# Kernel optimization log

Hardware: AMD Instinct MI355X
Metric: run time of the kernel (lower is better)

Reference implementation:

```python
import jax, jax.numpy as jnp
import numpy as np

IN_DIM = 128
LAYER_DIMS = [128, 128]
NUM_SAMPLES = [25, 10]
L0 = 3072
NEG_WEIGHT = 1.0


def setup_inputs() -> dict:
    key = jax.random.key(0)
    ks = jax.random.split(key, 12)
    feat = jax.random.normal(ks[0], (L0, IN_DIM), dtype=jnp.float32)
    nodes = jax.random.randint(ks[1], (L0,), 0, L0)
    nb0 = jnp.arange(L0)
    nb1 = jax.random.randint(ks[2], (L0 * 10,), 0, L0)
    nb2 = jax.random.randint(ks[3], (L0 * 10 * 25,), 0, L0)
    src_idx = jax.random.randint(ks[4], (1024,), 0, L0)
    pos_idx = jax.random.randint(ks[5], (1024,), 0, L0)
    neg_idx = jax.random.randint(ks[6], (512,), 0, L0)
    g = 0.05
    # mean aggregator weights: layer0 in=IN_DIM, layer1 in=2*128 (concat)
    w_self_0 = jax.random.normal(ks[7], (IN_DIM, 128), jnp.float32) * g
    w_neigh_0 = jax.random.normal(ks[8], (IN_DIM, 128), jnp.float32) * g
    w_self_1 = jax.random.normal(ks[9], (256, 128), jnp.float32) * g
    w_neigh_1 = jax.random.normal(ks[10], (256, 128), jnp.float32) * g
    return dict(nodes=nodes, feat=feat, src_idx=src_idx, pos_idx=pos_idx,
                neg_idx=neg_idx, nb0=nb0, nb1=nb1, nb2=nb2,
                w_self_0=w_self_0, w_neigh_0=w_neigh_0,
                w_self_1=w_self_1, w_neigh_1=w_neigh_1)


def _aggregate(hidden, params):
    # GraphSAGE layer stack: at layer l, combine each hop with the mean of its
    # sampled neighbors, concat self/neigh transforms, relu except last layer.
    num_layers = len(NUM_SAMPLES)
    for layer in range(num_layers):
        w_self, w_neigh = params[layer]
        is_last = layer == num_layers - 1
        next_hidden = []
        for hop in range(num_layers - layer):
            s = NUM_SAMPLES[num_layers - hop - 1]
            self_v = hidden[hop]  # [n, d]
            neigh = hidden[hop + 1].reshape(self_v.shape[0], s, self_v.shape[1])
            neigh_mean = jnp.mean(neigh, axis=1)
            h = jnp.concatenate([self_v @ w_self, neigh_mean @ w_neigh], axis=1)
            if not is_last:
                h = jax.nn.relu(h)
            next_hidden.append(h)
        hidden = next_hidden
    return hidden[0]


def _l2_normalize(x, eps=1e-12):
    return x * jax.lax.rsqrt(jnp.maximum(jnp.sum(x * x, axis=1, keepdims=True), eps))


def reference(nodes, feat, src_idx, pos_idx, neg_idx, nb0, nb1, nb2,
              w_self_0, w_neigh_0, w_self_1, w_neigh_1):
    hidden = [feat[nb0], feat[nb1], feat[nb2]]
    params = [(w_self_0, w_neigh_0), (w_self_1, w_neigh_1)]
    output = _aggregate(hidden, params)          # [L0, 256]
    output = _l2_normalize(output)
    src_emb = output[src_idx]                    # [B, 256]
    pos_emb = output[pos_idx]
    neg_emb = output[neg_idx]                    # [Nneg, 256]

    aff = jnp.sum(src_emb * pos_emb, axis=1)     # [B]
    neg_aff = src_emb @ neg_emb.T                # [B, Nneg]

    # MRR via double argsort (tf double top_k equivalent; ties -> positive last)
    aff_all = jnp.concatenate([neg_aff, aff[:, None]], axis=1)
    order = jnp.argsort(-aff_all, axis=1, stable=True)
    ranks = jnp.argsort(order, axis=1, stable=True)
    mrr = jnp.mean(1.0 / (ranks[:, -1].astype(jnp.float32) + 1.0))

    # sigmoid cross-entropy: labels 1 -> softplus(-x); labels 0 -> softplus(x)
    true_xent = jax.nn.softplus(-aff)
    neg_xent = jax.nn.softplus(neg_aff)
    loss = jnp.sum(true_xent) + NEG_WEIGHT * jnp.sum(neg_xent)
    loss = loss / jnp.asarray(src_emb.shape[0], jnp.float32)
    return src_emb, loss, mrr
```

## Files before the change

### kernel.cpp

```cpp
#include <hip/hip_runtime.h>
#include <math.h>

#define L0      3072
#define BATCH   1024
#define NNEG    512


__device__ __forceinline__ float bf2f(unsigned short u) {
  return __uint_as_float(((unsigned)u) << 16);
}
__device__ __forceinline__ void store_out(float v, float* p) { *p = v; }
__device__ __forceinline__ void store_out(float v, unsigned short* p) {
  unsigned x = __float_as_uint(v);
  *p = (unsigned short)((x + 0x7fff + ((x >> 16) & 1)) >> 16);
}

template<int K, int AW, int HOFF, bool NORM, typename OutT>
__global__ __launch_bounds__(512) void k_mm(
    const float* __restrict__ Ain,
    const float* __restrict__ W0, const float* __restrict__ W1,
    OutT* __restrict__ Out, const int ldo, const int outHalfOff) {
  __shared__ float AT[6 * AW];
  __shared__ float rs[8][3];
  const int t = threadIdx.x;
  const int base = blockIdx.x * 6;
  {
    const float4* __restrict__ src = (const float4*)(Ain + base * AW);
    float4* __restrict__ dst = (float4*)AT;
    for (int idx = t; idx < 6 * AW / 4; idx += 512) dst[idx] = src[idx];
  }
  __syncthreads();

  const int wave = t >> 6;
  const int half = wave >> 2;
  const int colg = (wave >> 1) & 1;
  const int rowg = wave & 1;
  const int rg = rowg * 3;
  const int col = colg * 64 + (t & 63);
  const float* __restrict__ W = (half ? W1 : W0) + col;
  const float* __restrict__ A0 = AT + rg * AW + half * HOFF;

  float acc[3] = {0.f, 0.f, 0.f};
#pragma unroll 4
  for (int d = 0; d < K; d += 4) {
    float4 a[3];
#pragma unroll
    for (int r = 0; r < 3; ++r) a[r] = *(const float4*)&A0[r * AW + d];
    float w[4];
#pragma unroll
    for (int i2 = 0; i2 < 4; ++i2) w[i2] = W[(d + i2) * 128];
#pragma unroll
    for (int i2 = 0; i2 < 4; ++i2)
#pragma unroll
      for (int r = 0; r < 3; ++r)
        acc[r] = fmaf(((const float*)&a[r])[i2], w[i2], acc[r]);
  }

  float scale[3] = {1.f, 1.f, 1.f};
  if (NORM) {
    float p[3];
#pragma unroll
    for (int r = 0; r < 3; ++r) p[r] = acc[r] * acc[r];
#pragma unroll
    for (int off = 32; off > 0; off >>= 1)
#pragma unroll
      for (int r = 0; r < 3; ++r) p[r] += __shfl_xor(p[r], off, 64);
    if ((t & 63) == 0) { rs[wave][0] = p[0]; rs[wave][1] = p[1]; rs[wave][2] = p[2]; }
    __syncthreads();
#pragma unroll
    for (int r = 0; r < 3; ++r) {
      const float s = rs[rowg][r] + rs[rowg + 2][r] + rs[rowg + 4][r] + rs[rowg + 6][r];
      scale[r] = rsqrtf(fmaxf(s, 1e-12f));
    }
  }
  OutT* __restrict__ O = Out + half * outHalfOff;
#pragma unroll
  for (int r = 0; r < 3; ++r)
    store_out(acc[r] * scale[r], &O[(base + rg + r) * ldo + col]);
}

__global__ __launch_bounds__(512) void k_aggmm(
    const unsigned short* __restrict__ X0, const unsigned short* __restrict__ Y0,
    const int* __restrict__ nb0, const int* __restrict__ nb1,
    const int* __restrict__ nb2,
    const float* __restrict__ ws1, const float* __restrict__ wn1,
    float* __restrict__ R) {
  __shared__ float gB[40][128], gC[40][128], gD[40][128];
  __shared__ float HT[4 * 512];
  __shared__ float rs[8][2];
  const int t = threadIdx.x;
  const int wave = t >> 6, lam = t & 63;
  const int base = blockIdx.x * 4;
  const int c8 = lam & 15, sub = lam >> 4;

#pragma unroll
  for (int k = 0; k < 5; ++k) {
    const int tau = wave + k * 8;
    const int li = tau / 10, j = tau - li * 10;
    const int r = (base + li) * 10 + j;
    int myidx = 0;
    if (lam < 25) myidx = nb2[r * 25 + lam];
    else if (lam == 25) myidx = nb1[r];

    float d8[8];
#pragma unroll
    for (int e = 0; e < 8; ++e) d8[e] = 0.f;
#pragma unroll
    for (int m = 0; m < 7; ++m) {
      const int kk = sub + 4 * m;
      const int ridx = __shfl(myidx, kk, 64);
      if (kk < 25) {
        const float4 raw = *(const float4*)(Y0 + ridx * 128 + c8 * 8);
        const unsigned short* u = (const unsigned short*)&raw;
#pragma unroll
        for (int e = 0; e < 8; ++e) d8[e] += bf2f(u[e]);
      }
    }
#pragma unroll
    for (int e = 0; e < 8; ++e) d8[e] += __shfl_xor(d8[e], 16, 64);
#pragma unroll
    for (int e = 0; e < 8; ++e) d8[e] += __shfl_xor(d8[e], 32, 64);

    const int r1 = __shfl(myidx, 25, 64);
    if (sub == 0) {
#pragma unroll
      for (int e = 0; e < 8; ++e) gD[tau][c8 * 8 + e] = fmaxf(d8[e] * 0.04f, 0.f);
      const float4 raw = *(const float4*)(Y0 + r1 * 128 + c8 * 8);
      const unsigned short* u = (const unsigned short*)&raw;
#pragma unroll
      for (int e = 0; e < 8; ++e) gB[tau][c8 * 8 + e] = bf2f(u[e]);
    } else if (sub == 1) {
      const float4 raw = *(const float4*)(X0 + r1 * 128 + c8 * 8);
      const unsigned short* u = (const unsigned short*)&raw;
#pragma unroll
      for (int e = 0; e < 8; ++e) gC[tau][c8 * 8 + e] = fmaxf(bf2f(u[e]), 0.f);
    }
  }
  __syncthreads();

  {
    const int li = t >> 7, c = t & 127;
    const int n0 = nb0[base + li];
    float sB = 0.f, sC = 0.f, sD = 0.f;
#pragma unroll
    for (int jj = 0; jj < 10; ++jj) {
      sB += gB[li * 10 + jj][c];
      sC += gC[li * 10 + jj][c];
      sD += gD[li * 10 + jj][c];
    }
    HT[li * 512 + c]       = fmaxf(bf2f(X0[n0 * 128 + c]), 0.f);
    HT[li * 512 + 128 + c] = fmaxf(sB * 0.1f, 0.f);
    HT[li * 512 + 256 + c] = sC * 0.1f;
    HT[li * 512 + 384 + c] = sD * 0.1f;
  }
  __syncthreads();

  const int half = wave >> 2;
  const int colg = (wave >> 1) & 1;
  const int rowg = wave & 1;
  const int rg = rowg * 2;
  const int col = colg * 64 + lam;
  const float* __restrict__ W = (half ? wn1 : ws1) + col;
  const float* __restrict__ A0 = HT + rg * 512 + half * 256;

  float acc[2] = {0.f, 0.f};
#pragma unroll 4
  for (int d = 0; d < 256; d += 4) {
    float4 a[2];
#pragma unroll
    for (int r = 0; r < 2; ++r) a[r] = *(const float4*)&A0[r * 512 + d];
    float w[4];
#pragma unroll
    for (int i2 = 0; i2 < 4; ++i2) w[i2] = W[(d + i2) * 128];
#pragma unroll
    for (int i2 = 0; i2 < 4; ++i2)
#pragma unroll
      for (int r = 0; r < 2; ++r)
        acc[r] = fmaf(((const float*)&a[r])[i2], w[i2], acc[r]);
  }

  float p[2];
#pragma unroll
  for (int r = 0; r < 2; ++r) p[r] = acc[r] * acc[r];
#pragma unroll
  for (int off = 32; off > 0; off >>= 1)
#pragma unroll
    for (int r = 0; r < 2; ++r) p[r] += __shfl_xor(p[r], off, 64);
  if (lam == 0) { rs[wave][0] = p[0]; rs[wave][1] = p[1]; }
  __syncthreads();
#pragma unroll
  for (int r = 0; r < 2; ++r) {
    const float s = rs[rowg][r] + rs[rowg + 2][r] + rs[rowg + 4][r] + rs[rowg + 6][r];
    const float scale = rsqrtf(fmaxf(s, 1e-12f));
    R[(base + rg + r) * 256 + half * 128 + col] = acc[r] * scale;
  }
}

__device__ __forceinline__ float softplusf(float x) {
  return fmaxf(x, 0.f) + log1pf(expf(-fabsf(x)));
}

__global__ __launch_bounds__(512) void k_neg(
    const float* __restrict__ O,
    const int* __restrict__ src_idx, const int* __restrict__ pos_idx,
    const int* __restrict__ neg_idx,
    float* __restrict__ out_src, int* __restrict__ rankPart,
    float* __restrict__ spPosPart, float* __restrict__ spNegPart) {
  __shared__ float SP[64 * 260];
  __shared__ float BT[256 * 64];
  __shared__ float affL[32];
  __shared__ int cntL[32];
  __shared__ float wsum[16];
  const int t = threadIdx.x;
  const int bid = blockIdx.x;
  const int rowBase = (bid >> 3) * 32;
  const int colBase = (bid & 7) * 64;
  const bool first = ((bid & 7) == 0);

  {
    const float4* __restrict__ s4 = (const float4*)O;
#pragma unroll
    for (int idx = t; idx < 64 * 64; idx += 512) {
      const int row = idx >> 6, c4 = idx & 63;
      const int rid = (row < 32) ? src_idx[rowBase + row]
                                 : pos_idx[rowBase + row - 32];
      *(float4*)&SP[row * 260 + c4 * 4] = s4[rid * 64 + c4];
    }
  }
  {
    const float4* __restrict__ s4 = (const float4*)O;
#pragma unroll
    for (int idx = t; idx < 64 * 64; idx += 512) {
      const int j = idx & 63, c4 = idx >> 6;
      const float4 v = s4[neg_idx[colBase + j] * 64 + c4];
      BT[(4 * c4 + 0) * 64 + j] = v.x;
      BT[(4 * c4 + 1) * 64 + j] = v.y;
      BT[(4 * c4 + 2) * 64 + j] = v.z;
      BT[(4 * c4 + 3) * 64 + j] = v.w;
    }
  }
  if (first) {
    const float4* __restrict__ s4 = (const float4*)O;
    float4* __restrict__ d4o = (float4*)out_src;
#pragma unroll
    for (int idx = t; idx < 32 * 64; idx += 512) {
      const int rr = idx >> 6, c4 = idx & 63;
      d4o[(rowBase + rr) * 64 + c4] = s4[src_idx[rowBase + rr] * 64 + c4];
    }
  }
  __syncthreads();

  const int tc = t & 31;
  const int rowg = t >> 5;
  const float* __restrict__ A0 = SP + rowg * 260;
  const float* __restrict__ A1 = SP + (rowg + 16) * 260;
  const float* __restrict__ SV = SP + t * 260;
  const float* __restrict__ PV = SP + (32 + t) * 260;

  float acc00 = 0.f, acc01 = 0.f, acc10 = 0.f, acc11 = 0.f, aff = 0.f;
#pragma unroll 4
  for (int d4 = 0; d4 < 64; ++d4) {
    const int dd = d4 * 4;
    const float4 a0 = *(const float4*)&A0[dd];
    const float4 a1 = *(const float4*)&A1[dd];
    float2 b[4];
#pragma unroll
    for (int i2 = 0; i2 < 4; ++i2)
      b[i2] = *(const float2*)&BT[(dd + i2) * 64 + 2 * tc];
    float4 sv, pv;
    if (t < 32) {
      sv = *(const float4*)&SV[dd];
      pv = *(const float4*)&PV[dd];
    }
#pragma unroll
    for (int i2 = 0; i2 < 4; ++i2) {
      const float va0 = ((const float*)&a0)[i2];
      const float va1 = ((const float*)&a1)[i2];
      acc00 = fmaf(va0, b[i2].x, acc00);
      acc01 = fmaf(va0, b[i2].y, acc01);
      acc10 = fmaf(va1, b[i2].x, acc10);
      acc11 = fmaf(va1, b[i2].y, acc11);
      if (t < 32)
        aff = fmaf(((const float*)&sv)[i2], ((const float*)&pv)[i2], aff);
    }
  }
  if (t < 32) affL[t] = aff;
  __syncthreads();

  float sp = softplusf(acc00) + softplusf(acc01) +
             softplusf(acc10) + softplusf(acc11);
  const float av0 = affL[rowg], av1 = affL[rowg + 16];
  int c0 = ((acc00 >= av0) ? 1 : 0) + ((acc01 >= av0) ? 1 : 0);
  int c1 = ((acc10 >= av1) ? 1 : 0) + ((acc11 >= av1) ? 1 : 0);
#pragma unroll
  for (int off = 16; off > 0; off >>= 1) {
    sp += __shfl_down(sp, off, 32);
    c0 += __shfl_down(c0, off, 32);
    c1 += __shfl_down(c1, off, 32);
  }
  if ((t & 31) == 0) {
    cntL[rowg] = c0;
    cntL[rowg + 16] = c1;
    wsum[rowg] = sp;
  }
  __syncthreads();

  if (t < 32) rankPart[(bid & 7) * 1024 + rowBase + t] = cntL[t];
  if (t == 0) {
    float sn = 0.f;
#pragma unroll
    for (int w = 0; w < 16; ++w) sn += wsum[w];
    spNegPart[bid] = sn;
  }
  if (first && t == 0) {
    float ps = 0.f;
#pragma unroll
    for (int r = 0; r < 32; ++r) ps += softplusf(-affL[r]);
    spPosPart[bid >> 3] = ps;
  }
}

__global__ __launch_bounds__(256) void k_finalize(
    const int* __restrict__ rankPart, const float* __restrict__ spPosPart,
    const float* __restrict__ spNegPart, float* __restrict__ out) {
  __shared__ float wa[4], wb[4];
  const int t = threadIdx.x;
  float s = 0.f;
  for (int i = t; i < BATCH; i += 256) {
    int rv = 0;
#pragma unroll
    for (int p = 0; p < 8; ++p) rv += rankPart[p * 1024 + i];
    s += 1.f / (float)(rv + 1);
  }
  float l = 0.f;
  if (t < 256) l += spNegPart[t];
  if (t < 32) l += spPosPart[t];
#pragma unroll
  for (int off = 32; off > 0; off >>= 1) {
    s += __shfl_down(s, off, 64);
    l += __shfl_down(l, off, 64);
  }
  if ((t & 63) == 0) { wa[t >> 6] = s; wb[t >> 6] = l; }
  __syncthreads();
  if (t == 0) {
    out[BATCH * 256]     = (wb[0] + wb[1] + wb[2] + wb[3]) * (1.f / 1024.f);
    out[BATCH * 256 + 1] = (wa[0] + wa[1] + wa[2] + wa[3]) * (1.f / 1024.f);
  }
}

extern "C" void kernel_launch(void* const* d_in, const int* in_sizes, int n_in,
                              void* d_out, int out_size, void* d_ws, size_t ws_size,
                              hipStream_t stream) {
  const float* feat   = (const float*)d_in[1];
  const int* src_idx  = (const int*)d_in[2];
  const int* pos_idx  = (const int*)d_in[3];
  const int* neg_idx  = (const int*)d_in[4];
  const int* nb0      = (const int*)d_in[5];
  const int* nb1      = (const int*)d_in[6];
  const int* nb2      = (const int*)d_in[7];
  const float* ws0    = (const float*)d_in[8];
  const float* wn0    = (const float*)d_in[9];
  const float* ws1    = (const float*)d_in[10];
  const float* wn1    = (const float*)d_in[11];

  float* wsf = (float*)d_ws;
  unsigned short* X0 = (unsigned short*)d_ws;
  unsigned short* Y0 = X0 + 393216;
  float* R       = wsf + 1966080;
  float* spPosP  = wsf + 2752512;
  float* spNegP  = wsf + 2752640;
  int*   rankP   = (int*)(wsf + 2753664);
  float* out     = (float*)d_out;

  k_mm<128, 128, 0, false, unsigned short><<<L0 / 6, 512, 0, stream>>>(
      feat, ws0, wn0, X0, 128, 393216);
  k_aggmm<<<L0 / 4, 512, 0, stream>>>(
      X0, Y0, nb0, nb1, nb2, ws1, wn1, R);
  k_neg<<<256, 512, 0, stream>>>(
      R, src_idx, pos_idx, neg_idx, out, rankP, spPosP, spNegP);
  k_finalize<<<1, 256, 0, stream>>>(rankP, spPosP, spNegP, out);
}
```

Before: 155.9 us.

## Accumulate neighbor sums in registers and swizzle negative-embedding transpose tile

The aggregation kernel now has each wave accumulate five hop-1 neighbor rows in registers and write only per-wave partial sums to shared memory. This replaces the 40-row staging arrays and the 10-way shared-memory reduction, cutting shared memory use and LDS traffic. Separately, the negative-embedding load in the scoring kernel is changed to coalesced row-major global reads. The transposed tile is stored with an XOR swizzle, and the matmul loop reads with the matching swizzled column to avoid bank conflicts.

```diff
diff --git a/kernel.cpp b/kernel.cpp
--- a/kernel.cpp
+++ b/kernel.cpp
@@ -85,7 +85,7 @@
     const int* __restrict__ nb2,
     const float* __restrict__ ws1, const float* __restrict__ wn1,
     float* __restrict__ R) {
-  __shared__ float gB[40][128], gC[40][128], gD[40][128];
+  __shared__ float pB[8][128], pC[8][128], pD[8][128];
   __shared__ float HT[4 * 512];
   __shared__ float rs[8][2];
   const int t = threadIdx.x;
@@ -93,47 +93,62 @@
   const int base = blockIdx.x * 4;
   const int c8 = lam & 15, sub = lam >> 4;
 
-#pragma unroll
-  for (int k = 0; k < 5; ++k) {
-    const int tau = wave + k * 8;
-    const int li = tau / 10, j = tau - li * 10;
-    const int r = (base + li) * 10 + j;
-    int myidx = 0;
-    if (lam < 25) myidx = nb2[r * 25 + lam];
-    else if (lam == 25) myidx = nb1[r];
-
-    float d8[8];
-#pragma unroll
-    for (int e = 0; e < 8; ++e) d8[e] = 0.f;
-#pragma unroll
-    for (int m = 0; m < 7; ++m) {
-      const int kk = sub + 4 * m;
-      const int ridx = __shfl(myidx, kk, 64);
-      if (kk < 25) {
-        const float4 raw = *(const float4*)(Y0 + ridx * 128 + c8 * 8);
+  {
+    const int li = wave >> 1;
+    const int j0 = (wave & 1) * 5;
+    float Ba[8], Ca[8], Da[8];
+#pragma unroll
+    for (int e = 0; e < 8; ++e) { Ba[e] = 0.f; Ca[e] = 0.f; Da[e] = 0.f; }
+#pragma unroll
+    for (int jj = 0; jj < 5; ++jj) {
+      const int r = (base + li) * 10 + j0 + jj;
+      int myidx = 0;
+      if (lam < 25) myidx = nb2[r * 25 + lam];
+      else if (lam == 25) myidx = nb1[r];
+
+      float d8[8];
+#pragma unroll
+      for (int e = 0; e < 8; ++e) d8[e] = 0.f;
+#pragma unroll
+      for (int m = 0; m < 7; ++m) {
+        const int kk = sub + 4 * m;
+        const int ridx = __shfl(myidx, kk, 64);
+        if (kk < 25) {
+          const float4 raw = *(const float4*)(Y0 + ridx * 128 + c8 * 8);
+          const unsigned short* u = (const unsigned short*)&raw;
+#pragma unroll
+          for (int e = 0; e < 8; ++e) d8[e] += bf2f(u[e]);
+        }
+      }
+#pragma unroll
+      for (int e = 0; e < 8; ++e) d8[e] += __shfl_xor(d8[e], 16, 64);
+#pragma unroll
+      for (int e = 0; e < 8; ++e) d8[e] += __shfl_xor(d8[e], 32, 64);
+#pragma unroll
+      for (int e = 0; e < 8; ++e) Da[e] += fmaxf(d8[e] * 0.04f, 0.f);
+
+      const int r1 = __shfl(myidx, 25, 64);
+      if (sub == 0) {
+        const float4 raw = *(const float4*)(Y0 + r1 * 128 + c8 * 8);
         const unsigned short* u = (const unsigned short*)&raw;
 #pragma unroll
-        for (int e = 0; e < 8; ++e) d8[e] += bf2f(u[e]);
+        for (int e = 0; e < 8; ++e) Ba[e] += bf2f(u[e]);
+      } else if (sub == 1) {
+        const float4 raw = *(const float4*)(X0 + r1 * 128 + c8 * 8);
+        const unsigned short* u = (const unsigned short*)&raw;
+#pragma unroll
+        for (int e = 0; e < 8; ++e) Ca[e] += fmaxf(bf2f(u[e]), 0.f);
       }
     }
-#pragma unroll
-    for (int e = 0; e < 8; ++e) d8[e] += __shfl_xor(d8[e], 16, 64);
-#pragma unroll
-    for (int e = 0; e < 8; ++e) d8[e] += __shfl_xor(d8[e], 32, 64);
-
-    const int r1 = __shfl(myidx, 25, 64);
     if (sub == 0) {
 #pragma unroll
-      for (int e = 0; e < 8; ++e) gD[tau][c8 * 8 + e] = fmaxf(d8[e] * 0.04f, 0.f);
-      const float4 raw = *(const float4*)(Y0 + r1 * 128 + c8 * 8);
-      const unsigned short* u = (const unsigned short*)&raw;
-#pragma unroll
-      for (int e = 0; e < 8; ++e) gB[tau][c8 * 8 + e] = bf2f(u[e]);
+      for (int e = 0; e < 8; ++e) {
+        pD[wave][c8 * 8 + e] = Da[e];
+        pB[wave][c8 * 8 + e] = Ba[e];
+      }
     } else if (sub == 1) {
-      const float4 raw = *(const float4*)(X0 + r1 * 128 + c8 * 8);
-      const unsigned short* u = (const unsigned short*)&raw;
-#pragma unroll
-      for (int e = 0; e < 8; ++e) gC[tau][c8 * 8 + e] = fmaxf(bf2f(u[e]), 0.f);
+#pragma unroll
+      for (int e = 0; e < 8; ++e) pC[wave][c8 * 8 + e] = Ca[e];
     }
   }
   __syncthreads();
@@ -141,13 +156,9 @@
   {
     const int li = t >> 7, c = t & 127;
     const int n0 = nb0[base + li];
-    float sB = 0.f, sC = 0.f, sD = 0.f;
-#pragma unroll
-    for (int jj = 0; jj < 10; ++jj) {
-      sB += gB[li * 10 + jj][c];
-      sC += gC[li * 10 + jj][c];
-      sD += gD[li * 10 + jj][c];
-    }
+    const float sB = pB[li * 2][c] + pB[li * 2 + 1][c];
+    const float sC = pC[li * 2][c] + pC[li * 2 + 1][c];
+    const float sD = pD[li * 2][c] + pD[li * 2 + 1][c];
     HT[li * 512 + c]       = fmaxf(bf2f(X0[n0 * 128 + c]), 0.f);
     HT[li * 512 + 128 + c] = fmaxf(sB * 0.1f, 0.f);
     HT[li * 512 + 256 + c] = sC * 0.1f;
@@ -231,12 +242,13 @@
     const float4* __restrict__ s4 = (const float4*)O;
 #pragma unroll
     for (int idx = t; idx < 64 * 64; idx += 512) {
-      const int j = idx & 63, c4 = idx >> 6;
+      const int j = idx >> 6, c4 = idx & 63;
       const float4 v = s4[neg_idx[colBase + j] * 64 + c4];
-      BT[(4 * c4 + 0) * 64 + j] = v.x;
-      BT[(4 * c4 + 1) * 64 + j] = v.y;
-      BT[(4 * c4 + 2) * 64 + j] = v.z;
-      BT[(4 * c4 + 3) * 64 + j] = v.w;
+      const int js = j ^ ((c4 & 31) << 1);
+      BT[(4 * c4 + 0) * 64 + js] = v.x;
+      BT[(4 * c4 + 1) * 64 + js] = v.y;
+      BT[(4 * c4 + 2) * 64 + js] = v.z;
+      BT[(4 * c4 + 3) * 64 + js] = v.w;
     }
   }
   if (first) {
@@ -261,12 +273,14 @@
 #pragma unroll 4
   for (int d4 = 0; d4 < 64; ++d4) {
     const int dd = d4 * 4;
+    const int g = (d4 & 31) << 1;
+    const int bcol = (2 * tc) ^ g;
     const float4 a0 = *(const float4*)&A0[dd];
     const float4 a1 = *(const float4*)&A1[dd];
     float2 b[4];
 #pragma unroll
     for (int i2 = 0; i2 < 4; ++i2)
-      b[i2] = *(const float2*)&BT[(dd + i2) * 64 + 2 * tc];
+      b[i2] = *(const float2*)&BT[(dd + i2) * 64 + bcol];
     float4 sv, pv;
     if (t < 32) {
       sv = *(const float4*)&SV[dd];
```

After: 168.2 us. 1.08x slower.
